# Performance work log

Measured on AMD Instinct MI355X. Metric: run time of the kernel, lower is better.

Reference implementation:

```python
import jax, jax.numpy as jnp
import numpy as np

HIDDEN = 2048
N_HEADS = 16
N_KV = 2
HEAD_DIM = HIDDEN // N_HEADS  # 128


def setup_inputs() -> dict:
    key = jax.random.key(0)
    ks = jax.random.split(key, 9)
    s = 0.02
    kv_dim = N_KV * HEAD_DIM
    return {
        "hidden_states": jax.random.normal(ks[0], (2, 2048, HIDDEN), jnp.float32),
        "Wq": jax.random.normal(ks[1], (HIDDEN, HIDDEN), jnp.float32) * s,
        "bq": jnp.zeros((HIDDEN,), jnp.float32),
        "Wk": jax.random.normal(ks[2], (HIDDEN, kv_dim), jnp.float32) * s,
        "bk": jnp.zeros((kv_dim,), jnp.float32),
        "Wv": jax.random.normal(ks[3], (HIDDEN, kv_dim), jnp.float32) * s,
        "bv": jnp.zeros((kv_dim,), jnp.float32),
        "Wo": jax.random.normal(ks[4], (HIDDEN, HIDDEN), jnp.float32) * s,
        "bo": jnp.zeros((HIDDEN,), jnp.float32),
    }


def reference(hidden_states, Wq, bq, Wk, bk, Wv, bv, Wo, bo):
    B, S, _ = hidden_states.shape
    scaling = HEAD_DIM ** (-0.5)
    rep = N_HEADS // N_KV

    q = hidden_states @ Wq + bq                      # [B,S,H*D]
    k = hidden_states @ Wk + bk                      # [B,S,KV*D]
    v = hidden_states @ Wv + bv

    q = q.reshape(B, S, N_HEADS, HEAD_DIM) * scaling
    k = k.reshape(B, S, N_KV, HEAD_DIM)
    v = v.reshape(B, S, N_KV, HEAD_DIM)
    # repeat_interleave KV heads to match query heads (faithful to source)
    k = jnp.repeat(k, rep, axis=2)                   # [B,S,H,D]
    v = jnp.repeat(v, rep, axis=2)

    attn = jnp.einsum('bqhd,bkhd->bhqk', q, k)       # [B,H,S,S] score matrix
    attn = jax.nn.softmax(attn, axis=-1)
    out = jnp.einsum('bhqk,bkhd->bqhd', attn, v)     # [B,S,H,D]
    out = out.reshape(B, S, N_HEADS * HEAD_DIM)
    return out @ Wo + bo
```

## Files before the change

kernel.cpp:

```cpp
#include <hip/hip_runtime.h>

typedef __bf16 bf16;
typedef __bf16 bf16x4 __attribute__((ext_vector_type(4)));
typedef __bf16 bf16x8 __attribute__((ext_vector_type(8)));
typedef float  f32x4  __attribute__((ext_vector_type(4)));

#define AS1 __attribute__((address_space(1)))
#define AS3 __attribute__((address_space(3)))

__device__ __forceinline__ void gload_lds16(const void* g, void* l) {
    __builtin_amdgcn_global_load_lds((const AS1 void*)g, (AS3 void*)l, 16, 0, 0);
}

__global__ __launch_bounds__(256) void prep(
    const float* __restrict__ X,  const float* __restrict__ Wq,
    const float* __restrict__ Wk, const float* __restrict__ Wv,
    const float* __restrict__ Wo, const float* __restrict__ bq,
    const float* __restrict__ bk, const float* __restrict__ bv,
    bf16* __restrict__ Xb, bf16* __restrict__ Wqkvt,
    bf16* __restrict__ Wot, float* __restrict__ bqkv)
{
    __shared__ float tile[32][33];
    int bid = blockIdx.x;
    if (bid < 8192) {
        int i = bid * 256 + threadIdx.x;
        float4 v = ((const float4*)X)[i];
        bf16x4 o = { (bf16)v.x, (bf16)v.y, (bf16)v.z, (bf16)v.w };
        ((bf16x4*)Xb)[i] = o;
        return;
    }
    bid -= 8192;
    const float* src; bf16* dst; int R, C, bx, by;
    if (bid < 4096)      { src = Wq; dst = Wqkvt;                      R = 2048; C = 2048; bx = bid & 63; by = bid >> 6; }
    else if (bid < 4608) { int t = bid - 4096; src = Wk; dst = Wqkvt + (size_t)2048 * 2048; R = 2048; C = 256; bx = t & 7; by = t >> 3; }
    else if (bid < 5120) { int t = bid - 4608; src = Wv; dst = Wqkvt + (size_t)2304 * 2048; R = 2048; C = 256; bx = t & 7; by = t >> 3; }
    else if (bid < 9216) { int t = bid - 5120; src = Wo; dst = Wot;    R = 2048; C = 2048; bx = t & 63; by = t >> 6; }
    else {
        int i = (bid - 9216) * 256 + threadIdx.x;
        if (i < 2048) bqkv[i] = bq[i];
        else if (i < 2304) bqkv[i] = bk[i - 2048];
        else if (i < 2560) bqkv[i] = bv[i - 2304];
        return;
    }
    int tx = threadIdx.x & 31, tg = threadIdx.x >> 5;
    int c0 = bx * 32, r0 = by * 32;
    #pragma unroll
    for (int j = tg; j < 32; j += 8)
        tile[j][tx] = src[(size_t)(r0 + j) * C + c0 + tx];
    __syncthreads();
    #pragma unroll
    for (int j = tg; j < 32; j += 8)
        dst[(size_t)(c0 + j) * R + r0 + tx] = (bf16)tile[tx][j];
}

template<int OUTBF>
__global__ __launch_bounds__(256) void gemm_bt(
    const bf16* __restrict__ A, const bf16* __restrict__ Bt,
    const float* __restrict__ bias, void* __restrict__ Cv,
    int M, int N, int K, float scale)
{
    __shared__ bf16 As[128 * 32];
    __shared__ bf16 Bs[128 * 32];
    const int tid = threadIdx.x;
    const int l = tid & 63, w = tid >> 6;
    const int wm = w >> 1, wn = w & 1;
    const size_t rowBase = (size_t)blockIdx.y * 128;
    const size_t colBase = (size_t)blockIdx.x * 128;

    f32x4 acc[4][4] = {};

    const int srow = l >> 2;
    const int schunk = (l & 3) ^ ((l >> 3) & 3);
    const int frow = l & 15;
    const int fswz = (frow >> 1) & 3;
    const int g = l >> 4;

    const bf16* Ag = A  + (rowBase + w * 32 + srow) * (size_t)K + schunk * 8;
    const bf16* Bg = Bt + (colBase + w * 32 + srow) * (size_t)K + schunk * 8;

    for (int k0 = 0; k0 < K; k0 += 32) {
        gload_lds16(Ag + k0,                  As + (w * 32) * 32);
        gload_lds16(Ag + 16 * (size_t)K + k0, As + (w * 32 + 16) * 32);
        gload_lds16(Bg + k0,                  Bs + (w * 32) * 32);
        gload_lds16(Bg + 16 * (size_t)K + k0, Bs + (w * 32 + 16) * 32);
        __syncthreads();

        bf16x8 af[4], bfr[4];
        #pragma unroll
        for (int mi = 0; mi < 4; ++mi)
            af[mi] = *(const bf16x8*)(As + (wm * 64 + mi * 16 + frow) * 32 + ((g ^ fswz) << 3));
        #pragma unroll
        for (int ni = 0; ni < 4; ++ni)
            bfr[ni] = *(const bf16x8*)(Bs + (wn * 64 + ni * 16 + frow) * 32 + ((g ^ fswz) << 3));
        #pragma unroll
        for (int mi = 0; mi < 4; ++mi)
            #pragma unroll
            for (int ni = 0; ni < 4; ++ni)
                acc[mi][ni] = __builtin_amdgcn_mfma_f32_16x16x32_bf16(af[mi], bfr[ni], acc[mi][ni], 0, 0, 0);
        __syncthreads();
    }

    const int cr = (l >> 4) * 4;
    const int cc = l & 15;
    #pragma unroll
    for (int ni = 0; ni < 4; ++ni) {
        const int col = (int)colBase + wn * 64 + ni * 16 + cc;
        const float bv = bias[col];
        #pragma unroll
        for (int mi = 0; mi < 4; ++mi) {
            #pragma unroll
            for (int r = 0; r < 4; ++r) {
                const size_t row = rowBase + wm * 64 + mi * 16 + cr + r;
                float v = (acc[mi][ni][r] + bv) * scale;
                if (OUTBF) ((bf16*)Cv)[row * N + col] = (bf16)v;
                else       ((float*)Cv)[row * N + col] = v;
            }
        }
    }
}

__global__ __launch_bounds__(256) void gemm_qkv(
    const bf16* __restrict__ A, const bf16* __restrict__ Bt,
    const float* __restrict__ bias, bf16* __restrict__ Qb, bf16* __restrict__ Kb,
    bf16* __restrict__ VT, float qscale)
{
    constexpr int K = 2048;
    __shared__ bf16 As[128 * 32];
    __shared__ bf16 Bs[128 * 32];
    const int tid = threadIdx.x;
    const int l = tid & 63, w = tid >> 6;
    const int wm = w >> 1, wn = w & 1;
    const size_t rowBase = (size_t)blockIdx.y * 128;
    const size_t colBase = (size_t)blockIdx.x * 128;

    f32x4 acc[4][4] = {};

    const int srow = l >> 2;
    const int schunk = (l & 3) ^ ((l >> 3) & 3);
    const int frow = l & 15;
    const int fswz = (frow >> 1) & 3;
    const int g = l >> 4;

    const bf16* Ag = A  + (rowBase + w * 32 + srow) * (size_t)K + schunk * 8;
    const bf16* Bg = Bt + (colBase + w * 32 + srow) * (size_t)K + schunk * 8;

    for (int k0 = 0; k0 < K; k0 += 32) {
        gload_lds16(Ag + k0,                  As + (w * 32) * 32);
        gload_lds16(Ag + 16 * (size_t)K + k0, As + (w * 32 + 16) * 32);
        gload_lds16(Bg + k0,                  Bs + (w * 32) * 32);
        gload_lds16(Bg + 16 * (size_t)K + k0, Bs + (w * 32 + 16) * 32);
        __syncthreads();

        bf16x8 af[4], bfr[4];
        #pragma unroll
        for (int mi = 0; mi < 4; ++mi)
            af[mi] = *(const bf16x8*)(As + (wm * 64 + mi * 16 + frow) * 32 + ((g ^ fswz) << 3));
        #pragma unroll
        for (int ni = 0; ni < 4; ++ni)
            bfr[ni] = *(const bf16x8*)(Bs + (wn * 64 + ni * 16 + frow) * 32 + ((g ^ fswz) << 3));
        #pragma unroll
        for (int mi = 0; mi < 4; ++mi)
            #pragma unroll
            for (int ni = 0; ni < 4; ++ni)
                acc[mi][ni] = __builtin_amdgcn_mfma_f32_16x16x32_bf16(af[mi], bfr[ni], acc[mi][ni], 0, 0, 0);
        __syncthreads();
    }

    const int cr = (l >> 4) * 4;
    const int cc = l & 15;
    const int cb = (int)colBase;
    #pragma unroll
    for (int ni = 0; ni < 4; ++ni) {
        const int col = cb + wn * 64 + ni * 16 + cc;
        const float bv = bias[col];
        if (cb < 2048) {
            #pragma unroll
            for (int mi = 0; mi < 4; ++mi)
                #pragma unroll
                for (int r = 0; r < 4; ++r) {
                    const size_t row = rowBase + wm * 64 + mi * 16 + cr + r;
                    Qb[row * 2048 + col] = (bf16)((acc[mi][ni][r] + bv) * qscale);
                }
        } else if (cb < 2304) {
            #pragma unroll
            for (int mi = 0; mi < 4; ++mi)
                #pragma unroll
                for (int r = 0; r < 4; ++r) {
                    const size_t row = rowBase + wm * 64 + mi * 16 + cr + r;
                    Kb[row * 256 + (col - 2048)] = (bf16)(acc[mi][ni][r] + bv);
                }
        } else {
            const int vcol = col - 2304;
            const int kvh = vcol >> 7, d = vcol & 127;
            #pragma unroll
            for (int mi = 0; mi < 4; ++mi) {
                const size_t row0 = rowBase + wm * 64 + mi * 16 + cr;
                const int bb = (int)(row0 >> 11);
                const int s  = (int)(row0 & 2047);
                const int tile = s >> 6, sp = s & 63;
                const int slot = (sp & 35) | ((sp & 8) << 1) | ((sp & 4) << 1) | ((sp & 16) >> 2);
                bf16x4 v4 = { (bf16)(acc[mi][ni][0] + bv), (bf16)(acc[mi][ni][1] + bv),
                              (bf16)(acc[mi][ni][2] + bv), (bf16)(acc[mi][ni][3] + bv) };
                *(bf16x4*)(VT + ((size_t)((bb * 2 + kvh) * 128 + d)) * 2048 + tile * 64 + slot) = v4;
            }
        }
    }
}

__global__ __launch_bounds__(512, 2) void attn_fwd(
    const bf16* __restrict__ Q, const bf16* __restrict__ Kb,
    const bf16* __restrict__ VT, bf16* __restrict__ O)
{
    constexpr int S = 2048;
    constexpr int NT = S / 64;
    extern __shared__ bf16 smem[];
    bf16* Ks = smem;
    bf16* Vs = smem + 16384;

    const int tid = threadIdx.x;
    const int l = tid & 63, w = tid >> 6;
    const int qt = blockIdx.x, h = blockIdx.y, b = blockIdx.z;
    const int kvh = h >> 3;
    const int lg = l >> 4, ll = l & 15;
    const int eh = (ll >> 2) & 1;

    bf16x8 qfA[4], qfB[4];
    {
        const bf16* qpA = Q + ((size_t)(b * S + qt * 256 + w * 32 + ll)) * 2048 + h * 128 + lg * 8;
        const bf16* qpB = qpA + 16 * 2048;
        #pragma unroll
        for (int j = 0; j < 4; ++j) {
            qfA[j] = *(const bf16x8*)(qpA + (j << 5));
            qfB[j] = *(const bf16x8*)(qpB + (j << 5));
        }
    }

    const bf16* Kg  = Kb + (size_t)b * S * 256 + kvh * 128;
    const bf16* VTg = VT + ((size_t)(b * 2 + kvh) * 128) * S;

    const bf16* kg0 = Kg + (size_t)(w * 8 + lg) * 256 + (ll ^ lg) * 8;
    const bf16* kg1 = Kg + (size_t)(w * 8 + 4 + lg) * 256 + (ll ^ (4 + lg)) * 8;
    const bf16* vg0 = VTg + (size_t)(w * 16 + (l >> 3)) * S + (((l & 7) ^ ((l >> 3) & 7)) << 3);
    const bf16* vg1 = vg0 + 8 * (size_t)S;
    const int kd0 = (w * 8) * 128;
    const int kd1 = (w * 8 + 4) * 128;
    const int vd0 = w * 1024;
    const int vd1 = w * 1024 + 512;

    const int swz8 = (lg ^ (ll & 3)) << 3;
    const int kbE = ll * 128 + swz8 + eh * 32;
    const int kbO = ll * 128 + swz8 + (1 - eh) * 32;
    const int vbE = ll * 64 + swz8 + eh * 32;
    const int vbO = ll * 64 + swz8 + (1 - eh) * 32;

    bf16x8 vones;
    #pragma unroll
    for (int e = 0; e < 8; ++e) vones[e] = (bf16)1.0f;

    f32x4 ofA[8] = {}, ofB[8] = {};
    f32x4 olA = {}, olB = {};
    bf16x8 pA0, pA1, pB0, pB1;

    gload_lds16(kg0, Ks + kd0);
    gload_lds16(kg1, Ks + kd1);
    gload_lds16(vg0, Vs + vd0);
    gload_lds16(vg1, Vs + vd1);
    __syncthreads();

    int sP = 2, sC = 0, sN = 1;
    for (int t = 0; t < NT; ++t) {
        const int buf = t & 1;
        if (t + 1 < NT) {
            const size_t ko = (size_t)(t + 1) * 64 * 256;
            const int    vo = (t + 1) * 64;
            gload_lds16(kg0 + ko, Ks + (buf ^ 1) * 8192 + kd0);
            gload_lds16(kg1 + ko, Ks + (buf ^ 1) * 8192 + kd1);
            gload_lds16(vg0 + vo, Vs + sN * 8192 + vd0);
            gload_lds16(vg1 + vo, Vs + sN * 8192 + vd1);
        }

        const bf16* kE = Ks + buf * 8192 + kbE;
        const bf16* kO = Ks + buf * 8192 + kbO;
        f32x4 scA[4] = {}, scB[4] = {};
        __builtin_amdgcn_s_setprio(1);
        #pragma unroll
        for (int ni = 0; ni < 4; ++ni) {
            bf16x8 k0f = *(const bf16x8*)(kE + ni * 2048);
            scA[ni] = __builtin_amdgcn_mfma_f32_16x16x32_bf16(k0f, qfA[0], scA[ni], 0, 0, 0);
            scB[ni] = __builtin_amdgcn_mfma_f32_16x16x32_bf16(k0f, qfB[0], scB[ni], 0, 0, 0);
            bf16x8 k1f = *(const bf16x8*)(kO + ni * 2048);
            scA[ni] = __builtin_amdgcn_mfma_f32_16x16x32_bf16(k1f, qfA[1], scA[ni], 0, 0, 0);
            scB[ni] = __builtin_amdgcn_mfma_f32_16x16x32_bf16(k1f, qfB[1], scB[ni], 0, 0, 0);
            bf16x8 k2f = *(const bf16x8*)(kE + ni * 2048 + 64);
            scA[ni] = __builtin_amdgcn_mfma_f32_16x16x32_bf16(k2f, qfA[2], scA[ni], 0, 0, 0);
            scB[ni] = __builtin_amdgcn_mfma_f32_16x16x32_bf16(k2f, qfB[2], scB[ni], 0, 0, 0);
            bf16x8 k3f = *(const bf16x8*)(kO + ni * 2048 + 64);
            scA[ni] = __builtin_amdgcn_mfma_f32_16x16x32_bf16(k3f, qfA[3], scA[ni], 0, 0, 0);
            scB[ni] = __builtin_amdgcn_mfma_f32_16x16x32_bf16(k3f, qfB[3], scB[ni], 0, 0, 0);
        }
        __builtin_amdgcn_s_setprio(0);

        if (t > 0) {
            const bf16* vE = Vs + sP * 8192 + vbE;
            const bf16* vO = Vs + sP * 8192 + vbO;
            __builtin_amdgcn_s_setprio(1);
            olA = __builtin_amdgcn_mfma_f32_16x16x32_bf16(pA0, vones, olA, 0, 0, 0);
            olB = __builtin_amdgcn_mfma_f32_16x16x32_bf16(pB0, vones, olB, 0, 0, 0);
            #pragma unroll
            for (int nf = 0; nf < 8; ++nf) {
                bf16x8 v0 = *(const bf16x8*)(vE + nf * 1024);
                ofA[nf] = __builtin_amdgcn_mfma_f32_16x16x32_bf16(pA0, v0, ofA[nf], 0, 0, 0);
                ofB[nf] = __builtin_amdgcn_mfma_f32_16x16x32_bf16(pB0, v0, ofB[nf], 0, 0, 0);
            }
            olA = __builtin_amdgcn_mfma_f32_16x16x32_bf16(pA1, vones, olA, 0, 0, 0);
            olB = __builtin_amdgcn_mfma_f32_16x16x32_bf16(pB1, vones, olB, 0, 0, 0);
            #pragma unroll
            for (int nf = 0; nf < 8; ++nf) {
                bf16x8 v1 = *(const bf16x8*)(vO + nf * 1024);
                ofA[nf] = __builtin_amdgcn_mfma_f32_16x16x32_bf16(pA1, v1, ofA[nf], 0, 0, 0);
                ofB[nf] = __builtin_amdgcn_mfma_f32_16x16x32_bf16(pB1, v1, ofB[nf], 0, 0, 0);
            }
            __builtin_amdgcn_s_setprio(0);
        }

        float pa[4][4], pb[4][4];
        #pragma unroll
        for (int ni = 0; ni < 4; ++ni)
            #pragma unroll
            for (int r = 0; r < 4; ++r) {
                pa[ni][r] = __builtin_exp2f(scA[ni][r]);
                pb[ni][r] = __builtin_exp2f(scB[ni][r]);
            }
        #pragma unroll
        for (int e = 0; e < 8; ++e) {
            pA0[e] = (bf16)pa[(e >> 2)][e & 3];
            pA1[e] = (bf16)pa[2 + (e >> 2)][e & 3];
            pB0[e] = (bf16)pb[(e >> 2)][e & 3];
            pB1[e] = (bf16)pb[2 + (e >> 2)][e & 3];
        }

        __syncthreads();
        int tmp = sP; sP = sC; sC = sN; sN = tmp;
    }

    {
        const bf16* vE = Vs + sP * 8192 + vbE;
        const bf16* vO = Vs + sP * 8192 + vbO;
        olA = __builtin_amdgcn_mfma_f32_16x16x32_bf16(pA0, vones, olA, 0, 0, 0);
        olB = __builtin_amdgcn_mfma_f32_16x16x32_bf16(pB0, vones, olB, 0, 0, 0);
        #pragma unroll
        for (int nf = 0; nf < 8; ++nf) {
            bf16x8 v0 = *(const bf16x8*)(vE + nf * 1024);
            ofA[nf] = __builtin_amdgcn_mfma_f32_16x16x32_bf16(pA0, v0, ofA[nf], 0, 0, 0);
            ofB[nf] = __builtin_amdgcn_mfma_f32_16x16x32_bf16(pB0, v0, ofB[nf], 0, 0, 0);
        }
        olA = __builtin_amdgcn_mfma_f32_16x16x32_bf16(pA1, vones, olA, 0, 0, 0);
        olB = __builtin_amdgcn_mfma_f32_16x16x32_bf16(pB1, vones, olB, 0, 0, 0);
        #pragma unroll
        for (int nf = 0; nf < 8; ++nf) {
            bf16x8 v1 = *(const bf16x8*)(vO + nf * 1024);
            ofA[nf] = __builtin_amdgcn_mfma_f32_16x16x32_bf16(pA1, v1, ofA[nf], 0, 0, 0);
            ofB[nf] = __builtin_amdgcn_mfma_f32_16x16x32_bf16(pB1, v1, ofB[nf], 0, 0, 0);
        }
    }

    #pragma unroll
    for (int r = 0; r < 4; ++r) {
        float invA = 1.0f / olA[r];
        float invB = 1.0f / olB[r];
        size_t rowA = (size_t)(b * S + qt * 256 + w * 32 + lg * 4 + r);
        bf16* opA = O + rowA * 2048 + h * 128 + ll;
        bf16* opB = opA + 16 * 2048;
        #pragma unroll
        for (int nf = 0; nf < 8; ++nf) {
            opA[nf * 16] = (bf16)(ofA[nf][r] * invA);
            opB[nf * 16] = (bf16)(ofB[nf][r] * invB);
        }
    }
}

extern "C" void kernel_launch(void* const* d_in, const int* in_sizes, int n_in,
                              void* d_out, int out_size, void* d_ws, size_t ws_size,
                              hipStream_t stream)
{
    const float* X  = (const float*)d_in[0];
    const float* Wq = (const float*)d_in[1];
    const float* bq = (const float*)d_in[2];
    const float* Wk = (const float*)d_in[3];
    const float* bk = (const float*)d_in[4];
    const float* Wv = (const float*)d_in[5];
    const float* bv = (const float*)d_in[6];
    const float* Wo = (const float*)d_in[7];
    const float* bo = (const float*)d_in[8];
    float* out = (float*)d_out;

    bf16* p = (bf16*)d_ws;
    bf16* Xb    = p; p += 8388608;
    bf16* Qb    = p; p += 8388608;
    bf16* Kbuf  = p; p += 1048576;
    bf16* VTb   = p; p += 1048576;
    bf16* Wqkvt = p; p += 5242880;
    bf16* Wot   = p; p += 4194304;
    float* bqkv = (float*)p; p += 5120;
    bf16* Oattn = Xb;

    const float qscale = 0.12751744f;

    (void)hipFuncSetAttribute((const void*)attn_fwd,
                              hipFuncAttributeMaxDynamicSharedMemorySize, 81920);

    prep<<<17418, 256, 0, stream>>>(X, Wq, Wk, Wv, Wo, bq, bk, bv,
                                    Xb, Wqkvt, Wot, bqkv);

    gemm_qkv<<<dim3(20, 32), 256, 0, stream>>>(Xb, Wqkvt, bqkv, Qb, Kbuf, VTb, qscale);

    attn_fwd<<<dim3(8, 16, 2), 512, 81920, stream>>>(Qb, Kbuf, VTb, Oattn);

    gemm_bt<0><<<dim3(16, 32), 256, 0, stream>>>(Oattn, Wot, bo, out, 4096, 2048, 2048, 1.0f);
}
```

Before: 200.5 us.

## Halve attention block size to 4 waves with 128 query rows each

The attention kernel now runs 256-thread blocks covering 128 query rows instead of 512-thread blocks covering 256, and launches twice as many blocks. Each thread issues twice as many async global-to-LDS loads per K/V tile so the shared tile is still filled by fewer waves. The aim is better scheduling across CUs with more, smaller blocks. In exchange, the same K/V tiles are loaded twice as often overall, and each tile has fewer waves to reuse it.

New measurement: 199.0 us. No clear change (-0.8%).

```diff
diff --git a/kernel.cpp b/kernel.cpp
--- a/kernel.cpp
+++ b/kernel.cpp
@@ -207,7 +207,7 @@
     }
 }
 
-__global__ __launch_bounds__(512, 2) void attn_fwd(
+__global__ __launch_bounds__(256, 2) void attn_fwd(
     const bf16* __restrict__ Q, const bf16* __restrict__ Kb,
     const bf16* __restrict__ VT, bf16* __restrict__ O)
 {
@@ -226,7 +226,7 @@
 
     bf16x8 qfA[4], qfB[4];
     {
-        const bf16* qpA = Q + ((size_t)(b * S + qt * 256 + w * 32 + ll)) * 2048 + h * 128 + lg * 8;
+        const bf16* qpA = Q + ((size_t)(b * S + qt * 128 + w * 32 + ll)) * 2048 + h * 128 + lg * 8;
         const bf16* qpB = qpA + 16 * 2048;
         #pragma unroll
         for (int j = 0; j < 4; ++j) {
@@ -238,14 +238,12 @@
     const bf16* Kg  = Kb + (size_t)b * S * 256 + kvh * 128;
     const bf16* VTg = VT + ((size_t)(b * 2 + kvh) * 128) * S;
 
-    const bf16* kg0 = Kg + (size_t)(w * 8 + lg) * 256 + (ll ^ lg) * 8;
-    const bf16* kg1 = Kg + (size_t)(w * 8 + 4 + lg) * 256 + (ll ^ (4 + lg)) * 8;
-    const bf16* vg0 = VTg + (size_t)(w * 16 + (l >> 3)) * S + (((l & 7) ^ ((l >> 3) & 7)) << 3);
-    const bf16* vg1 = vg0 + 8 * (size_t)S;
-    const int kd0 = (w * 8) * 128;
-    const int kd1 = (w * 8 + 4) * 128;
-    const int vd0 = w * 1024;
-    const int vd1 = w * 1024 + 512;
+    const bf16* kgA = Kg + (size_t)(w * 16 + lg) * 256 + (ll ^ lg) * 8;
+    const bf16* kgB = Kg + (size_t)(w * 16 + 4 + lg) * 256 + (ll ^ (4 + lg)) * 8;
+    const bf16* vgA = VTg + (size_t)(w * 32 + (l >> 3)) * S + (((l & 7) ^ ((l >> 3) & 7)) << 3);
+    const int kdA = (w * 16) * 128;
+    const int kdB = (w * 16 + 4) * 128;
+    const int vdA = w * 2048;
 
     const int swz8 = (lg ^ (ll & 3)) << 3;
     const int kbE = ll * 128 + swz8 + eh * 32;
@@ -261,10 +259,19 @@
     f32x4 olA = {}, olB = {};
     bf16x8 pA0, pA1, pB0, pB1;
 
-    gload_lds16(kg0, Ks + kd0);
-    gload_lds16(kg1, Ks + kd1);
-    gload_lds16(vg0, Vs + vd0);
-    gload_lds16(vg1, Vs + vd1);
+#define STAGE(koff, vroff, kbuf, vslot)                                   \
+    {                                                                     \
+        gload_lds16(kgA + (koff),             Ks + (kbuf) * 8192 + kdA);  \
+        gload_lds16(kgB + (koff),             Ks + (kbuf) * 8192 + kdB);  \
+        gload_lds16(kgA + (koff) + 2048,      Ks + (kbuf) * 8192 + kdA + 1024); \
+        gload_lds16(kgB + (koff) + 2048,      Ks + (kbuf) * 8192 + kdB + 1024); \
+        gload_lds16(vgA + (vroff),            Vs + (vslot) * 8192 + vdA);       \
+        gload_lds16(vgA + (vroff) + 8  * S,   Vs + (vslot) * 8192 + vdA + 512); \
+        gload_lds16(vgA + (vroff) + 16 * S,   Vs + (vslot) * 8192 + vdA + 1024);\
+        gload_lds16(vgA + (vroff) + 24 * S,   Vs + (vslot) * 8192 + vdA + 1536);\
+    }
+
+    STAGE(0, 0, 0, 0)
     __syncthreads();
 
     int sP = 2, sC = 0, sN = 1;
@@ -273,10 +280,7 @@
         if (t + 1 < NT) {
             const size_t ko = (size_t)(t + 1) * 64 * 256;
             const int    vo = (t + 1) * 64;
-            gload_lds16(kg0 + ko, Ks + (buf ^ 1) * 8192 + kd0);
-            gload_lds16(kg1 + ko, Ks + (buf ^ 1) * 8192 + kd1);
-            gload_lds16(vg0 + vo, Vs + sN * 8192 + vd0);
-            gload_lds16(vg1 + vo, Vs + sN * 8192 + vd1);
+            STAGE(ko, vo, buf ^ 1, sN)
         }
 
         const bf16* kE = Ks + buf * 8192 + kbE;
@@ -368,7 +372,7 @@
     for (int r = 0; r < 4; ++r) {
         float invA = 1.0f / olA[r];
         float invB = 1.0f / olB[r];
-        size_t rowA = (size_t)(b * S + qt * 256 + w * 32 + lg * 4 + r);
+        size_t rowA = (size_t)(b * S + qt * 128 + w * 32 + lg * 4 + r);
         bf16* opA = O + rowA * 2048 + h * 128 + ll;
         bf16* opB = opA + 16 * 2048;
         #pragma unroll
@@ -377,6 +381,7 @@
             opB[nf * 16] = (bf16)(ofB[nf][r] * invB);
         }
     }
+#undef STAGE
 }
 
 extern "C" void kernel_launch(void* const* d_in, const int* in_sizes, int n_in,
@@ -414,7 +419,7 @@
 
     gemm_qkv<<<dim3(20, 32), 256, 0, stream>>>(Xb, Wqkvt, bqkv, Qb, Kbuf, VTb, qscale);
 
-    attn_fwd<<<dim3(8, 16, 2), 512, 81920, stream>>>(Qb, Kbuf, VTb, Oattn);
+    attn_fwd<<<dim3(16, 16, 2), 256, 81920, stream>>>(Qb, Kbuf, VTb, Oattn);
 
     gemm_bt<0><<<dim3(16, 32), 256, 0, stream>>>(Oattn, Wot, bo, out, 4096, 2048, 2048, 1.0f);
 }
```
